# Kernel optimization log

Measured on AMD Instinct MI355X. Metric: run time of the kernel, lower is better.

Reference implementation:

```python
import jax, jax.numpy as jnp
import numpy as np

N, E, F, DE, G, C = 50000, 800000, 64, 32, 512, 2
EPS = 1e-5


def setup_inputs() -> dict:
    key = jax.random.key(0)
    ks = jax.random.split(key, 12)
    Z = 2 * F + DE  # CGConv concat dim [x_i, x_j, edge_attr]
    inp = {
        "x": jax.random.normal(ks[0], (N, F), dtype=jnp.float32),
        "edge_index": jax.random.randint(ks[1], (2, E), 0, N, dtype=jnp.int32),
        "edge_attr": jax.random.normal(ks[2], (E, DE), dtype=jnp.float32),
        "batch": jnp.sort(jax.random.randint(ks[3], (N,), 0, G, dtype=jnp.int32)),
        # CGConv lin_f / lin_s : (2F+De) -> F, with bias
        "Wf": jax.random.normal(ks[4], (Z, F), dtype=jnp.float32) * 0.05,
        "bf": jnp.zeros((F,), dtype=jnp.float32),
        "Ws": jax.random.normal(ks[5], (Z, F), dtype=jnp.float32) * 0.05,
        "bs": jnp.zeros((F,), dtype=jnp.float32),
        # CGConv internal BatchNorm (training-mode batch stats)
        "bn_w": jnp.ones((F,), dtype=jnp.float32),
        "bn_b": jnp.zeros((F,), dtype=jnp.float32),
        # PyG LayerNorm (graph mode, batch=None -> whole-tensor stats)
        "ln_w": jnp.ones((F,), dtype=jnp.float32),
        "ln_b": jnp.zeros((F,), dtype=jnp.float32),
        # final linear (2F -> C) and output LayerNorm
        "Wl": jax.random.normal(ks[6], (2 * F, C), dtype=jnp.float32) * 0.05,
        "bl": jnp.zeros((C,), dtype=jnp.float32),
        "ln4_w": jnp.ones((C,), dtype=jnp.float32),
        "ln4_b": jnp.zeros((C,), dtype=jnp.float32),
    }
    return inp


def _pyg_layernorm(x, w, b):
    # torch_geometric.nn.LayerNorm, mode='graph', batch=None: whole-tensor stats
    xc = x - jnp.mean(x)
    out = xc / (jnp.sqrt(jnp.mean(xc * xc)) + EPS)
    return out * w + b


def reference(x, edge_index, edge_attr, batch, Wf, bf, Ws, bs, bn_w, bn_b,
              ln_w, ln_b, Wl, bl, ln4_w, ln4_b):
    src = edge_index[0]  # x_j (source)
    dst = edge_index[1]  # x_i (target / aggregation index)

    # CGConv message: sigmoid(lin_f(z)) * softplus(lin_s(z)), z=[x_i,x_j,e]
    z = jnp.concatenate([x[dst], x[src], edge_attr], axis=1)  # [E, 2F+De]
    msg = jax.nn.sigmoid(z @ Wf + bf) * jax.nn.softplus(z @ Ws + bs)  # [E,F]

    # scatter-add aggregation to target nodes
    agg = jax.ops.segment_sum(msg, dst, num_segments=N)  # [N,F]

    # CGConv batch_norm=True (training-mode batch statistics over nodes)
    mu = jnp.mean(agg, axis=0)
    var = jnp.mean((agg - mu) ** 2, axis=0)
    agg = (agg - mu) / jnp.sqrt(var + EPS) * bn_w + bn_b

    # residual
    h = agg + x

    # LayerNorm + softplus
    h = jax.nn.softplus(_pyg_layernorm(h, ln_w, ln_b))

    # global mean / add pooling over graphs
    add_pool = jax.ops.segment_sum(h, batch, num_segments=G)  # [G,F]
    counts = jax.ops.segment_sum(jnp.ones((N,), h.dtype), batch, num_segments=G)
    mean_pool = add_pool / jnp.maximum(counts, 1.0)[:, None]

    g = jnp.concatenate([mean_pool, add_pool], axis=1)  # [G, 2F]
    out = g @ Wl + bl  # [G, C]
    out = _pyg_layernorm(out, ln4_w, ln4_b)
    return out
```

## Files before the change

kernel.cpp:

```cpp
#include <hip/hip_runtime.h>
#include <math.h>

#define EPSF 1e-5f

__global__ __launch_bounds__(256) void node_gemm(
    const float* __restrict__ x, const float* __restrict__ Wf,
    const float* __restrict__ bf, const float* __restrict__ Ws,
    const float* __restrict__ bs, float* __restrict__ Pdst,
    float* __restrict__ Psrc, int N) {
  const int lane = threadIdx.x & 63;
  const int w = threadIdx.x >> 6;
  const float* W = (w & 1) ? Ws : Wf;
  const int baseRow = (w >> 1) * 64;
  float wreg[64];
#pragma unroll
  for (int k = 0; k < 64; ++k) wreg[k] = W[(baseRow + k) * 64 + lane];
  float bias = 0.f;
  if (w == 0) bias = bf[lane];
  if (w == 1) bias = bs[lane];
  float* outp = (w >> 1) ? Psrc : Pdst;
  const int outOff = (w & 1) * 64;

  for (int n = blockIdx.x; n < N; n += gridDim.x) {
    const float* xr = x + (size_t)n * 64;
    float acc = bias;
#pragma unroll
    for (int k = 0; k < 64; k += 4) {
      float4 xv = *(const float4*)(xr + k);
      acc = fmaf(xv.x, wreg[k], acc);
      acc = fmaf(xv.y, wreg[k + 1], acc);
      acc = fmaf(xv.z, wreg[k + 2], acc);
      acc = fmaf(xv.w, wreg[k + 3], acc);
    }
    outp[(size_t)n * 128 + outOff + lane] = acc;
  }
}

__global__ __launch_bounds__(512) void wT_kernel(const float* __restrict__ Wf,
                                                 const float* __restrict__ Ws,
                                                 float4* __restrict__ WfT4,
                                                 float4* __restrict__ WsT4) {
  const int t = threadIdx.x, g = t >> 6, l = t & 63;
  const int k = 128 + 4 * g;
  WfT4[g * 64 + l] = make_float4(Wf[k * 64 + l], Wf[(k + 1) * 64 + l],
                                 Wf[(k + 2) * 64 + l], Wf[(k + 3) * 64 + l]);
  WsT4[g * 64 + l] = make_float4(Ws[k * 64 + l], Ws[(k + 1) * 64 + l],
                                 Ws[(k + 2) * 64 + l], Ws[(k + 3) * 64 + l]);
}

__global__ void hist_kernel(const int* __restrict__ ei, int* __restrict__ deg,
                            int E) {
  int i = blockIdx.x * blockDim.x + threadIdx.x;
  if (i < E) atomicAdd(&deg[ei[E + i]], 1);
}

__global__ __launch_bounds__(256) void scan_a(const int* __restrict__ deg,
                                              int* __restrict__ bsum, int N) {
  const int idx = blockIdx.x * 256 + threadIdx.x;
  int v = (idx < N) ? deg[idx] : 0;
#pragma unroll
  for (int o = 32; o > 0; o >>= 1) v += __shfl_down(v, o);
  __shared__ int ws4[4];
  if ((threadIdx.x & 63) == 0) ws4[threadIdx.x >> 6] = v;
  __syncthreads();
  if (threadIdx.x == 0) bsum[blockIdx.x] = ws4[0] + ws4[1] + ws4[2] + ws4[3];
}

__global__ __launch_bounds__(256) void scan_b(const int* __restrict__ bsum,
                                              int* __restrict__ bpre, int NB) {
  const int t = threadIdx.x;
  const int lane = t & 63, w = t >> 6;
  int v = (t < NB) ? bsum[t] : 0;
  int sc = v;
#pragma unroll
  for (int o = 1; o < 64; o <<= 1) {
    int u = __shfl_up(sc, o);
    if (lane >= o) sc += u;
  }
  __shared__ int wsum[4];
  if (lane == 63) wsum[w] = sc;
  __syncthreads();
  int add = 0;
#pragma unroll
  for (int k = 0; k < 4; ++k) add += (k < w) ? wsum[k] : 0;
  bpre[t] = (sc - v) + add;
}

__global__ __launch_bounds__(256) void scan_c(const int* __restrict__ deg,
                                              const int* __restrict__ bpre,
                                              int* __restrict__ offsets,
                                              int* __restrict__ cursor, int N) {
  const int t = threadIdx.x;
  const int lane = t & 63, w = t >> 6;
  const int idx = blockIdx.x * 256 + t;
  int d = (idx < N) ? deg[idx] : 0;
  int sc = d;
#pragma unroll
  for (int o = 1; o < 64; o <<= 1) {
    int u = __shfl_up(sc, o);
    if (lane >= o) sc += u;
  }
  __shared__ int wsum[4];
  if (lane == 63) wsum[w] = sc;
  __syncthreads();
  int add = bpre[blockIdx.x];
#pragma unroll
  for (int k = 0; k < 4; ++k) add += (k < w) ? wsum[k] : 0;
  const int off = add + (sc - d);
  if (idx < N) {
    offsets[idx] = off;
    cursor[idx] = off;
    if (idx == N - 1) offsets[N] = off + d;
  }
}

__global__ void scatter_kernel(const int* __restrict__ ei,
                               int* __restrict__ cursor,
                               int2* __restrict__ epair, int E) {
  int i = blockIdx.x * blockDim.x + threadIdx.x;
  if (i < E) {
    int dst = ei[E + i];
    int pos = atomicAdd(&cursor[dst], 1);
    epair[pos] = make_int2(i, ei[i]);
  }
}

__global__ __launch_bounds__(256, 5) void edge_agg(
    const int* __restrict__ offsets, const int2* __restrict__ epair,
    const float* __restrict__ eattr, const float4* __restrict__ WfT4,
    const float4* __restrict__ WsT4, const float* __restrict__ Pdst,
    const float* __restrict__ Psrc, float* __restrict__ agg, int N) {
  const int lane = threadIdx.x & 63;
  const int n = blockIdx.x * 4 + (threadIdx.x >> 6);
  if (n >= N) return;
  const int o0 = offsets[n];
  const int o1 = offsets[n + 1];
  const float fb = Pdst[(size_t)n * 128 + lane];
  const float sb = Pdst[(size_t)n * 128 + 64 + lane];
  float acc = 0.f;
  for (int base = o0; base < o1; base += 64) {
    const int m = min(64, o1 - base);
    int2 p = make_int2(0, 0);
    if (lane < m) p = epair[base + lane];
    for (int j = 0; j < m; ++j) {
      const int ex = __builtin_amdgcn_readlane(p.x, j);
      const int sr = __builtin_amdgcn_readlane(p.y, j);
      const float* er = eattr + (size_t)ex * 32;
      const float* pr = Psrc + (size_t)sr * 128;
      float fA0 = fb + pr[lane], fA1 = 0.f, fA2 = 0.f, fA3 = 0.f;
      float sA0 = sb + pr[64 + lane], sA1 = 0.f, sA2 = 0.f, sA3 = 0.f;
#pragma unroll
      for (int g = 0; g < 8; g += 4) {
        float4 e0 = *(const float4*)(er + 4 * g);
        float4 e1 = *(const float4*)(er + 4 * g + 4);
        float4 e2 = *(const float4*)(er + 4 * g + 8);
        float4 e3 = *(const float4*)(er + 4 * g + 12);
        float4 w0 = WfT4[(g + 0) * 64 + lane];
        float4 w1 = WfT4[(g + 1) * 64 + lane];
        float4 w2 = WfT4[(g + 2) * 64 + lane];
        float4 w3 = WfT4[(g + 3) * 64 + lane];
        float4 v0 = WsT4[(g + 0) * 64 + lane];
        float4 v1 = WsT4[(g + 1) * 64 + lane];
        float4 v2 = WsT4[(g + 2) * 64 + lane];
        float4 v3 = WsT4[(g + 3) * 64 + lane];
        fA0 = fmaf(e0.x, w0.x, fA0); fA0 = fmaf(e0.y, w0.y, fA0);
        fA0 = fmaf(e0.z, w0.z, fA0); fA0 = fmaf(e0.w, w0.w, fA0);
        fA1 = fmaf(e1.x, w1.x, fA1); fA1 = fmaf(e1.y, w1.y, fA1);
        fA1 = fmaf(e1.z, w1.z, fA1); fA1 = fmaf(e1.w, w1.w, fA1);
        fA2 = fmaf(e2.x, w2.x, fA2); fA2 = fmaf(e2.y, w2.y, fA2);
        fA2 = fmaf(e2.z, w2.z, fA2); fA2 = fmaf(e2.w, w2.w, fA2);
        fA3 = fmaf(e3.x, w3.x, fA3); fA3 = fmaf(e3.y, w3.y, fA3);
        fA3 = fmaf(e3.z, w3.z, fA3); fA3 = fmaf(e3.w, w3.w, fA3);
        sA0 = fmaf(e0.x, v0.x, sA0); sA0 = fmaf(e0.y, v0.y, sA0);
        sA0 = fmaf(e0.z, v0.z, sA0); sA0 = fmaf(e0.w, v0.w, sA0);
        sA1 = fmaf(e1.x, v1.x, sA1); sA1 = fmaf(e1.y, v1.y, sA1);
        sA1 = fmaf(e1.z, v1.z, sA1); sA1 = fmaf(e1.w, v1.w, sA1);
        sA2 = fmaf(e2.x, v2.x, sA2); sA2 = fmaf(e2.y, v2.y, sA2);
        sA2 = fmaf(e2.z, v2.z, sA2); sA2 = fmaf(e2.w, v2.w, sA2);
        sA3 = fmaf(e3.x, v3.x, sA3); sA3 = fmaf(e3.y, v3.y, sA3);
        sA3 = fmaf(e3.z, v3.z, sA3); sA3 = fmaf(e3.w, v3.w, sA3);
      }
      float f = (fA0 + fA1) + (fA2 + fA3);
      float s = (sA0 + sA1) + (sA2 + sA3);
      float sig = __builtin_amdgcn_rcpf(1.0f + __expf(-f));
      float sp = fmaxf(s, 0.f) + __logf(1.0f + __expf(-fabsf(s)));
      acc += sig * sp;
    }
  }
  agg[(size_t)n * 64 + lane] = acc;
}

__global__ __launch_bounds__(256) void stats_kernel(
    const float* __restrict__ agg, const float* __restrict__ x,
    float* __restrict__ stats, int N) {
  const int f = threadIdx.x & 63;
  const int sub = threadIdx.x >> 6;
  float sa = 0, sa2 = 0, sx = 0, sx2 = 0, sax = 0;
  for (int r = blockIdx.x * 4 + sub; r < N; r += gridDim.x * 4) {
    float a = agg[(size_t)r * 64 + f];
    float xv = x[(size_t)r * 64 + f];
    sa += a; sa2 += a * a; sx += xv; sx2 += xv * xv; sax += a * xv;
  }
  __shared__ float lds[4][5][64];
  lds[sub][0][f] = sa; lds[sub][1][f] = sa2; lds[sub][2][f] = sx;
  lds[sub][3][f] = sx2; lds[sub][4][f] = sax;
  __syncthreads();
  if (sub == 0) {
#pragma unroll
    for (int i = 0; i < 5; ++i) {
      float v = lds[0][i][f] + lds[1][i][f] + lds[2][i][f] + lds[3][i][f];
      atomicAdd(&stats[i * 64 + f], v);
    }
  }
}

__global__ __launch_bounds__(64) void finalize_stats(
    const float* __restrict__ stats, const float* __restrict__ bn_w,
    const float* __restrict__ bn_b, float* __restrict__ ab, int N) {
  const int f = threadIdx.x;
  const float Nf = (float)N;
  const float invN = 1.0f / Nf;
  float Sa = stats[f], Sa2 = stats[64 + f], Sx = stats[128 + f],
        Sx2 = stats[192 + f], Sax = stats[256 + f];
  float mu = Sa * invN;
  float var = Sa2 * invN - mu * mu;
  float alpha = bn_w[f] / sqrtf(var + EPSF);
  float beta = bn_b[f] - mu * alpha;
  float Sh = alpha * Sa + Nf * beta + Sx;
  float Sh2 = alpha * alpha * Sa2 + Sx2 + Nf * beta * beta +
              2.f * alpha * Sax + 2.f * alpha * beta * Sa + 2.f * beta * Sx;
#pragma unroll
  for (int o = 32; o > 0; o >>= 1) {
    Sh += __shfl_down(Sh, o);
    Sh2 += __shfl_down(Sh2, o);
  }
  ab[f] = alpha;
  ab[64 + f] = beta;
  if (f == 0) {
    float cnt = Nf * 64.0f;
    float mean = Sh / cnt;
    float msq = Sh2 / cnt - mean * mean;
    ab[128] = mean;
    ab[129] = 1.0f / (sqrtf(fmaxf(msq, 0.f)) + EPSF);
  }
}

__global__ __launch_bounds__(256) void node_finish(
    const float* __restrict__ agg, const float* __restrict__ x,
    const int* __restrict__ batch, const float* __restrict__ ab,
    const float* __restrict__ ln_w, const float* __restrict__ ln_b,
    float* __restrict__ add_pool, float* __restrict__ counts, int N,
    int chunk) {
  const int f = threadIdx.x & 63;
  const int sub = threadIdx.x >> 6;
  const int r0 = blockIdx.x * chunk;
  const int r1 = min(N, r0 + chunk);
  const float alpha = ab[f], beta = ab[64 + f];
  const float mean = ab[128], rden = ab[129];
  const float lw = ln_w[f] * rden;
  const float lb = ln_b[f];
  float acc = 0.f, cacc = 0.f;
  int curg = -1;
  for (int r = r0 + sub; r < r1; r += 4) {
    int g = batch[r];
    if (g != curg) {
      if (curg >= 0) {
        atomicAdd(&add_pool[(size_t)curg * 64 + f], acc);
        if (f == 0) atomicAdd(&counts[curg], cacc);
      }
      curg = g; acc = 0.f; cacc = 0.f;
    }
    float h = fmaf(alpha, agg[(size_t)r * 64 + f], beta) + x[(size_t)r * 64 + f];
    float v = (h - mean) * lw + lb;
    float sp = fmaxf(v, 0.f) + __logf(1.0f + __expf(-fabsf(v)));
    acc += sp; cacc += 1.f;
  }
  if (curg >= 0) {
    atomicAdd(&add_pool[(size_t)curg * 64 + f], acc);
    if (f == 0) atomicAdd(&counts[curg], cacc);
  }
}

__global__ __launch_bounds__(1024) void graph_out(
    const float* __restrict__ add_pool, const float* __restrict__ counts,
    const float* __restrict__ Wl, const float* __restrict__ bl,
    const float* __restrict__ w4, const float* __restrict__ b4,
    float* __restrict__ out, int G) {
  const int t = threadIdx.x;
  const int g = t >> 1, c = t & 1;
  float cnt = fmaxf(counts[g], 1.0f);
  float inv = 1.0f / cnt;
  const float* ap = add_pool + (size_t)g * 64;
  float v = bl[c];
#pragma unroll 8
  for (int k = 0; k < 64; ++k)
    v = fmaf(ap[k], fmaf(Wl[k * 2 + c], inv, Wl[(64 + k) * 2 + c]), v);

  __shared__ float red[16];
  __shared__ float bc[2];
  float sum = v;
#pragma unroll
  for (int o = 32; o > 0; o >>= 1) sum += __shfl_down(sum, o);
  if ((t & 63) == 0) red[t >> 6] = sum;
  __syncthreads();
  if (t == 0) {
    float tot = 0;
#pragma unroll
    for (int i = 0; i < 16; ++i) tot += red[i];
    bc[0] = tot * (1.0f / 1024.0f);
  }
  __syncthreads();
  const float mean = bc[0];
  const float xc = v - mean;
  float sq = xc * xc;
  __syncthreads();
#pragma unroll
  for (int o = 32; o > 0; o >>= 1) sq += __shfl_down(sq, o);
  if ((t & 63) == 0) red[t >> 6] = sq;
  __syncthreads();
  if (t == 0) {
    float tot = 0;
#pragma unroll
    for (int i = 0; i < 16; ++i) tot += red[i];
    bc[1] = 1.0f / (sqrtf(tot * (1.0f / 1024.0f)) + EPSF);
  }
  __syncthreads();
  out[t] = xc * bc[1] * w4[c] + b4[c];
}

extern "C" void kernel_launch(void* const* d_in, const int* in_sizes, int n_in,
                              void* d_out, int out_size, void* d_ws,
                              size_t ws_size, hipStream_t stream) {
  const float* x = (const float*)d_in[0];
  const int* ei = (const int*)d_in[1];
  const float* eattr = (const float*)d_in[2];
  const int* batch = (const int*)d_in[3];
  const float* Wf = (const float*)d_in[4];
  const float* bf = (const float*)d_in[5];
  const float* Ws = (const float*)d_in[6];
  const float* bs = (const float*)d_in[7];
  const float* bn_w = (const float*)d_in[8];
  const float* bn_b = (const float*)d_in[9];
  const float* ln_w = (const float*)d_in[10];
  const float* ln_b = (const float*)d_in[11];
  const float* Wl = (const float*)d_in[12];
  const float* bl = (const float*)d_in[13];
  const float* w4 = (const float*)d_in[14];
  const float* b4 = (const float*)d_in[15];

  const int N = in_sizes[0] / 64;
  const int E = in_sizes[2] / 32;
  const int G = 512;
  const int NB = (N + 255) / 256;

  float* ws = (float*)d_ws;
  float* agg = ws;
  int* offsets = (int*)(agg + (size_t)N * 64);
  float* stats = (float*)(offsets + N + 4);
  float* add_pool = stats + 320;
  float* counts = add_pool + (size_t)G * 64;
  int* deg = (int*)(counts + G);
  int* cursor = deg + N;
  float* ab = (float*)(cursor + N);
  int* bsum = (int*)(ab + 132);
  int* bpre = bsum + 256;
  float4* WfT4 = (float4*)(bpre + 256);
  float4* WsT4 = WfT4 + 512;
  int2* epair = (int2*)(WsT4 + 512);
  float* Pdst = (float*)((int*)epair + 2 * (size_t)E);
  float* Psrc = Pdst + (size_t)N * 128;

  size_t zeroFloats = 320 + (size_t)G * 64 + G + N;
  hipMemsetAsync(stats, 0, zeroFloats * sizeof(float), stream);

  node_gemm<<<1024, 256, 0, stream>>>(x, Wf, bf, Ws, bs, Pdst, Psrc, N);
  wT_kernel<<<1, 512, 0, stream>>>(Wf, Ws, WfT4, WsT4);
  hist_kernel<<<(E + 255) / 256, 256, 0, stream>>>(ei, deg, E);
  scan_a<<<NB, 256, 0, stream>>>(deg, bsum, N);
  scan_b<<<1, 256, 0, stream>>>(bsum, bpre, NB);
  scan_c<<<NB, 256, 0, stream>>>(deg, bpre, offsets, cursor, N);
  scatter_kernel<<<(E + 255) / 256, 256, 0, stream>>>(ei, cursor, epair, E);
  edge_agg<<<(N + 3) / 4, 256, 0, stream>>>(offsets, epair, eattr, WfT4, WsT4,
                                            Pdst, Psrc, agg, N);
  stats_kernel<<<512, 256, 0, stream>>>(agg, x, stats, N);
  finalize_stats<<<1, 64, 0, stream>>>(stats, bn_w, bn_b, ab, N);
  const int chunk = (N + 511) / 512;
  node_finish<<<512, 256, 0, stream>>>(agg, x, batch, ab, ln_w, ln_b, add_pool,
                                       counts, N, chunk);
  graph_out<<<1, 1024, 0, stream>>>(add_pool, counts, Wl, bl, w4, b4,
                                    (float*)d_out, G);
}
```

Baseline: 368.4 us.

## Compute edge-attribute projection with bf16 MFMA over edge tiles

Replaces the per-node wavefront edge loop with an edge-parallel kernel. Each block takes 64 dst-sorted edges, converts their edge attributes to bf16 and computes the edge_attr×W products with 16x16x32 bf16 MFMA instructions. Messages are run-length reduced per destination in LDS and then atomically added to the global aggregate, which is now zeroed by an enlarged memset. This removes the scalar FMA work and the load imbalance across high-degree nodes, at the cost of bf16 rounding of edge features and weights, global atomics at tile boundaries, and wider int4 edge records.

```diff
diff --git a/kernel.cpp b/kernel.cpp
--- a/kernel.cpp
+++ b/kernel.cpp
@@ -2,6 +2,15 @@
 #include <math.h>
 
 #define EPSF 1e-5f
+
+typedef short bf16x8 __attribute__((ext_vector_type(8)));
+typedef float f32x4 __attribute__((ext_vector_type(4)));
+
+static __device__ __forceinline__ unsigned short f2bf(float x) {
+  unsigned u = __float_as_uint(x);
+  unsigned r = (u + 0x7FFFu + ((u >> 16) & 1u)) >> 16;
+  return (unsigned short)r;
+}
 
 __global__ __launch_bounds__(256) void node_gemm(
     const float* __restrict__ x, const float* __restrict__ Wf,
@@ -36,16 +45,18 @@
   }
 }
 
-__global__ __launch_bounds__(512) void wT_kernel(const float* __restrict__ Wf,
-                                                 const float* __restrict__ Ws,
-                                                 float4* __restrict__ WfT4,
-                                                 float4* __restrict__ WsT4) {
-  const int t = threadIdx.x, g = t >> 6, l = t & 63;
-  const int k = 128 + 4 * g;
-  WfT4[g * 64 + l] = make_float4(Wf[k * 64 + l], Wf[(k + 1) * 64 + l],
-                                 Wf[(k + 2) * 64 + l], Wf[(k + 3) * 64 + l]);
-  WsT4[g * 64 + l] = make_float4(Ws[k * 64 + l], Ws[(k + 1) * 64 + l],
-                                 Ws[(k + 2) * 64 + l], Ws[(k + 3) * 64 + l]);
+__global__ __launch_bounds__(512) void bfrag_kernel(
+    const float* __restrict__ Wf, const float* __restrict__ Ws,
+    unsigned short* __restrict__ Bfrag) {
+  const int l = threadIdx.x & 63, t8 = threadIdx.x >> 6;
+  const int q = l & 15, g = l >> 4;
+  const float* W = (t8 < 4) ? Wf : Ws;
+  const int col = (t8 & 3) * 16 + q;
+  unsigned short out[8];
+#pragma unroll
+  for (int i = 0; i < 8; ++i)
+    out[i] = f2bf(W[(size_t)(128 + g * 8 + i) * 64 + col]);
+  *(uint4*)&Bfrag[((size_t)t8 * 64 + l) * 8] = *(uint4*)out;
 }
 
 __global__ void hist_kernel(const int* __restrict__ ei, int* __restrict__ deg,
@@ -116,78 +127,126 @@
 
 __global__ void scatter_kernel(const int* __restrict__ ei,
                                int* __restrict__ cursor,
-                               int2* __restrict__ epair, int E) {
+                               int4* __restrict__ epair4, int E) {
   int i = blockIdx.x * blockDim.x + threadIdx.x;
   if (i < E) {
     int dst = ei[E + i];
     int pos = atomicAdd(&cursor[dst], 1);
-    epair[pos] = make_int2(i, ei[i]);
-  }
-}
-
-__global__ __launch_bounds__(256, 5) void edge_agg(
-    const int* __restrict__ offsets, const int2* __restrict__ epair,
-    const float* __restrict__ eattr, const float4* __restrict__ WfT4,
-    const float4* __restrict__ WsT4, const float* __restrict__ Pdst,
-    const float* __restrict__ Psrc, float* __restrict__ agg, int N) {
-  const int lane = threadIdx.x & 63;
-  const int n = blockIdx.x * 4 + (threadIdx.x >> 6);
-  if (n >= N) return;
-  const int o0 = offsets[n];
-  const int o1 = offsets[n + 1];
-  const float fb = Pdst[(size_t)n * 128 + lane];
-  const float sb = Pdst[(size_t)n * 128 + 64 + lane];
-  float acc = 0.f;
-  for (int base = o0; base < o1; base += 64) {
-    const int m = min(64, o1 - base);
-    int2 p = make_int2(0, 0);
-    if (lane < m) p = epair[base + lane];
-    for (int j = 0; j < m; ++j) {
-      const int ex = __builtin_amdgcn_readlane(p.x, j);
-      const int sr = __builtin_amdgcn_readlane(p.y, j);
-      const float* er = eattr + (size_t)ex * 32;
-      const float* pr = Psrc + (size_t)sr * 128;
-      float fA0 = fb + pr[lane], fA1 = 0.f, fA2 = 0.f, fA3 = 0.f;
-      float sA0 = sb + pr[64 + lane], sA1 = 0.f, sA2 = 0.f, sA3 = 0.f;
-#pragma unroll
-      for (int g = 0; g < 8; g += 4) {
-        float4 e0 = *(const float4*)(er + 4 * g);
-        float4 e1 = *(const float4*)(er + 4 * g + 4);
-        float4 e2 = *(const float4*)(er + 4 * g + 8);
-        float4 e3 = *(const float4*)(er + 4 * g + 12);
-        float4 w0 = WfT4[(g + 0) * 64 + lane];
-        float4 w1 = WfT4[(g + 1) * 64 + lane];
-        float4 w2 = WfT4[(g + 2) * 64 + lane];
-        float4 w3 = WfT4[(g + 3) * 64 + lane];
-        float4 v0 = WsT4[(g + 0) * 64 + lane];
-        float4 v1 = WsT4[(g + 1) * 64 + lane];
-        float4 v2 = WsT4[(g + 2) * 64 + lane];
-        float4 v3 = WsT4[(g + 3) * 64 + lane];
-        fA0 = fmaf(e0.x, w0.x, fA0); fA0 = fmaf(e0.y, w0.y, fA0);
-        fA0 = fmaf(e0.z, w0.z, fA0); fA0 = fmaf(e0.w, w0.w, fA0);
-        fA1 = fmaf(e1.x, w1.x, fA1); fA1 = fmaf(e1.y, w1.y, fA1);
-        fA1 = fmaf(e1.z, w1.z, fA1); fA1 = fmaf(e1.w, w1.w, fA1);
-        fA2 = fmaf(e2.x, w2.x, fA2); fA2 = fmaf(e2.y, w2.y, fA2);
-        fA2 = fmaf(e2.z, w2.z, fA2); fA2 = fmaf(e2.w, w2.w, fA2);
-        fA3 = fmaf(e3.x, w3.x, fA3); fA3 = fmaf(e3.y, w3.y, fA3);
-        fA3 = fmaf(e3.z, w3.z, fA3); fA3 = fmaf(e3.w, w3.w, fA3);
-        sA0 = fmaf(e0.x, v0.x, sA0); sA0 = fmaf(e0.y, v0.y, sA0);
-        sA0 = fmaf(e0.z, v0.z, sA0); sA0 = fmaf(e0.w, v0.w, sA0);
-        sA1 = fmaf(e1.x, v1.x, sA1); sA1 = fmaf(e1.y, v1.y, sA1);
-        sA1 = fmaf(e1.z, v1.z, sA1); sA1 = fmaf(e1.w, v1.w, sA1);
-        sA2 = fmaf(e2.x, v2.x, sA2); sA2 = fmaf(e2.y, v2.y, sA2);
-        sA2 = fmaf(e2.z, v2.z, sA2); sA2 = fmaf(e2.w, v2.w, sA2);
-        sA3 = fmaf(e3.x, v3.x, sA3); sA3 = fmaf(e3.y, v3.y, sA3);
-        sA3 = fmaf(e3.z, v3.z, sA3); sA3 = fmaf(e3.w, v3.w, sA3);
-      }
-      float f = (fA0 + fA1) + (fA2 + fA3);
-      float s = (sA0 + sA1) + (sA2 + sA3);
-      float sig = __builtin_amdgcn_rcpf(1.0f + __expf(-f));
-      float sp = fmaxf(s, 0.f) + __logf(1.0f + __expf(-fabsf(s)));
-      acc += sig * sp;
+    epair4[pos] = make_int4(i, ei[i], dst, 0);
+  }
+}
+
+__global__ __launch_bounds__(256) void edge_mfma(
+    const int4* __restrict__ epair4, const float* __restrict__ eattr,
+    const unsigned short* __restrict__ Bfrag, const float* __restrict__ Pdst,
+    const float* __restrict__ Psrc, float* __restrict__ agg, int E, int N) {
+  __shared__ __align__(16) unsigned short Ash[64 * 40];
+  __shared__ __align__(16) int sd[128];
+  __shared__ int eidx[64];
+  __shared__ __align__(4) unsigned char ridb[64];
+  __shared__ int rdst[64];
+  __shared__ int nruns_s;
+  __shared__ float msum[64][66];
+
+  const int t = threadIdx.x, lane = t & 63, w = t >> 6;
+  const int q = lane & 15, g = lane >> 4;
+  const int base = blockIdx.x * 64;
+
+  if (w == 0) {
+    const int eg = base + lane;
+    int4 p = make_int4(0, 0, 0, 0);
+    if (eg < E) p = epair4[eg];
+    const int valid = (eg < E);
+    sd[lane * 2] = valid ? p.y : 0;
+    sd[lane * 2 + 1] = valid ? p.z : 0;
+    eidx[lane] = valid ? p.x : 0;
+    int d = valid ? p.z : 0x7FFFFFFF;
+    int dprev = __shfl_up(d, 1);
+    int flag = (lane == 0 || d != dprev) ? 1 : 0;
+    int sc = flag;
+#pragma unroll
+    for (int o = 1; o < 64; o <<= 1) {
+      int u = __shfl_up(sc, o);
+      if (lane >= o) sc += u;
     }
-  }
-  agg[(size_t)n * 64 + lane] = acc;
+    int rid = sc - 1;
+    ridb[lane] = (unsigned char)rid;
+    if (flag) rdst[rid] = d;
+    if (lane == 63) nruns_s = sc;
+  }
+  for (int i = t; i < 64 * 66; i += 256) ((float*)msum)[i] = 0.f;
+  __syncthreads();
+
+  {
+    const int row = t >> 2, c = t & 3;
+    const float* er = eattr + (size_t)eidx[row] * 32 + c * 8;
+    float4 v0 = *(const float4*)er;
+    float4 v1 = *(const float4*)(er + 4);
+    bf16x8 sv;
+    sv[0] = (short)f2bf(v0.x); sv[1] = (short)f2bf(v0.y);
+    sv[2] = (short)f2bf(v0.z); sv[3] = (short)f2bf(v0.w);
+    sv[4] = (short)f2bf(v1.x); sv[5] = (short)f2bf(v1.y);
+    sv[6] = (short)f2bf(v1.z); sv[7] = (short)f2bf(v1.w);
+    *(bf16x8*)&Ash[row * 40 + c * 8] = sv;
+  }
+  __syncthreads();
+
+  union U { uint4 u; bf16x8 v; };
+  bf16x8 b[8];
+#pragma unroll
+  for (int i = 0; i < 8; ++i) {
+    U uu;
+    uu.u = ((const uint4*)Bfrag)[i * 64 + lane];
+    b[i] = uu.v;
+  }
+  const bf16x8 a = *(const bf16x8*)&Ash[(q + 16 * w) * 40 + g * 8];
+  f32x4 acc[8];
+#pragma unroll
+  for (int i = 0; i < 8; ++i) {
+    f32x4 z = {0.f, 0.f, 0.f, 0.f};
+    acc[i] = __builtin_amdgcn_mfma_f32_16x16x32_bf16(a, b[i], z, 0, 0, 0);
+  }
+
+  const int e0 = 16 * w + g * 4;
+  int4 lo = *(const int4*)&sd[e0 * 2];
+  int4 hi = *(const int4*)&sd[e0 * 2 + 4];
+  const unsigned rid4 = *(const unsigned*)&ridb[e0];
+  const float* pdp[4] = {Pdst + (size_t)lo.y * 128, Pdst + (size_t)lo.w * 128,
+                         Pdst + (size_t)hi.y * 128, Pdst + (size_t)hi.w * 128};
+  const float* psp[4] = {Psrc + (size_t)lo.x * 128, Psrc + (size_t)lo.z * 128,
+                         Psrc + (size_t)hi.x * 128, Psrc + (size_t)hi.z * 128};
+  const int r0 = rid4 & 255, r1 = (rid4 >> 8) & 255, r2 = (rid4 >> 16) & 255,
+            r3 = (rid4 >> 24) & 255;
+
+#pragma unroll
+  for (int t8 = 0; t8 < 4; ++t8) {
+    const int feat = t8 * 16 + q;
+    float mm[4];
+#pragma unroll
+    for (int reg = 0; reg < 4; ++reg) {
+      float Ff = acc[t8][reg] + pdp[reg][feat] + psp[reg][feat];
+      float Fs = acc[t8 + 4][reg] + pdp[reg][64 + feat] + psp[reg][64 + feat];
+      float sig = __builtin_amdgcn_rcpf(1.0f + __expf(-Ff));
+      float sp = fmaxf(Fs, 0.f) + __logf(1.0f + __expf(-fabsf(Fs)));
+      mm[reg] = sig * sp;
+    }
+    float a_ = mm[0];
+    int cur = r0;
+    if (r1 == cur) a_ += mm[1];
+    else { atomicAdd(&msum[cur][feat], a_); cur = r1; a_ = mm[1]; }
+    if (r2 == cur) a_ += mm[2];
+    else { atomicAdd(&msum[cur][feat], a_); cur = r2; a_ = mm[2]; }
+    if (r3 == cur) a_ += mm[3];
+    else { atomicAdd(&msum[cur][feat], a_); cur = r3; a_ = mm[3]; }
+    atomicAdd(&msum[cur][feat], a_);
+  }
+  __syncthreads();
+
+  const int nr = nruns_s;
+  for (int r = w; r < nr; r += 4) {
+    const int dn = rdst[r];
+    if (dn < N) atomicAdd(&agg[(size_t)dn * 64 + lane], msum[r][lane]);
+  }
 }
 
 __global__ __launch_bounds__(256) void stats_kernel(
@@ -352,6 +411,7 @@
   const int E = in_sizes[2] / 32;
   const int G = 512;
   const int NB = (N + 255) / 256;
+  const int T = (E + 63) / 64;
 
   float* ws = (float*)d_ws;
   float* agg = ws;
@@ -364,24 +424,23 @@
   float* ab = (float*)(cursor + N);
   int* bsum = (int*)(ab + 132);
   int* bpre = bsum + 256;
-  float4* WfT4 = (float4*)(bpre + 256);
-  float4* WsT4 = WfT4 + 512;
-  int2* epair = (int2*)(WsT4 + 512);
-  float* Pdst = (float*)((int*)epair + 2 * (size_t)E);
+  unsigned short* Bfrag = (unsigned short*)(bpre + 256);
+  int4* epair4 = (int4*)((int*)(bpre + 256) + 2048);
+  float* Pdst = (float*)((int*)epair4 + 4 * (size_t)E);
   float* Psrc = Pdst + (size_t)N * 128;
 
-  size_t zeroFloats = 320 + (size_t)G * 64 + G + N;
-  hipMemsetAsync(stats, 0, zeroFloats * sizeof(float), stream);
+  size_t zeroFloats =
+      (size_t)N * 64 + (N + 4) + 320 + (size_t)G * 64 + G + N;
+  hipMemsetAsync(agg, 0, zeroFloats * sizeof(float), stream);
 
   node_gemm<<<1024, 256, 0, stream>>>(x, Wf, bf, Ws, bs, Pdst, Psrc, N);
-  wT_kernel<<<1, 512, 0, stream>>>(Wf, Ws, WfT4, WsT4);
+  bfrag_kernel<<<1, 512, 0, stream>>>(Wf, Ws, Bfrag);
   hist_kernel<<<(E + 255) / 256, 256, 0, stream>>>(ei, deg, E);
   scan_a<<<NB, 256, 0, stream>>>(deg, bsum, N);
   scan_b<<<1, 256, 0, stream>>>(bsum, bpre, NB);
   scan_c<<<NB, 256, 0, stream>>>(deg, bpre, offsets, cursor, N);
-  scatter_kernel<<<(E + 255) / 256, 256, 0, stream>>>(ei, cursor, epair, E);
-  edge_agg<<<(N + 3) / 4, 256, 0, stream>>>(offsets, epair, eattr, WfT4, WsT4,
-                                            Pdst, Psrc, agg, N);
+  scatter_kernel<<<(E + 255) / 256, 256, 0, stream>>>(ei, cursor, epair4, E);
+  edge_mfma<<<T, 256, 0, stream>>>(epair4, eattr, Bfrag, Pdst, Psrc, agg, E, N);
   stats_kernel<<<512, 256, 0, stream>>>(agg, x, stats, N);
   finalize_stats<<<1, 64, 0, stream>>>(stats, bn_w, bn_b, ab, N);
   const int chunk = (N + 511) / 512;
```

Result: faster. 332.5 us (-9.7%).
